# Performance work log

Hardware: AMD Instinct MI355X
Metric: run time of the kernel (lower is better)

Reference implementation:

```python
import jax, jax.numpy as jnp
import numpy as np

IN_FEATURES = 8192
OUT_FEATURES = 8192
W_BITS = 4
SCALE = float(2 ** 16)


def pbatch_round_quantize(W, n, scale=SCALE):
    """Faithful jnp port of pbatch_round_quantize.

    The torch module decomposes this quantized matrix into bitplanes packed
    into int32 words and accumulates scale_b * (bitplane @ x); the sum of the
    bitplane contributions is exactly (quantized / scale), so we compute that
    directly.
    """
    W_sign = jnp.sign(W)
    W_fixed = jnp.trunc(W * scale)            # (W * scale).astype(int), trunc toward 0
    v = jnp.abs(W_fixed)
    m = jnp.max(v)
    max_place = jnp.maximum(jnp.ceil(jnp.log2(m)) + 1.0, float(n))
    step = jnp.exp2(max_place - n)            # 2 ** (max_place - n)
    # mask = ((1<<max_place)-1) & ~(step-1) == 2**max_place - step
    mask = jnp.exp2(max_place) - step
    # bins[x] = mask - x*step (decreasing, uniformly spaced); centers are midpoints.
    # np.digitize(v, centers) for decreasing centers counts centers > v:
    #   idx = ceil((mask - v)/step - 0.5); then min(len(centers)-1, idx).
    if n == 1:
        # excl_zero: single bin, centers == bins, index always 0
        j = jnp.zeros_like(v)
    else:
        n_centers = 2 ** n - 1
        idx = jnp.ceil((mask - v) / step - 0.5)
        j = jnp.clip(idx, 0.0, float(n_centers - 1))
    rounded = W_sign * (mask - j * step)
    return rounded / scale


def setup_inputs() -> dict:
    key = jax.random.key(0)
    k_in, k_w, k_b = jax.random.split(key, 3)
    input = jax.random.normal(k_in, (IN_FEATURES,), dtype=jnp.float32)
    # reset_parameters: weight = randn(out, in)
    weight = jax.random.normal(k_w, (OUT_FEATURES, IN_FEATURES), dtype=jnp.float32)
    bound = 1.0 / np.sqrt(IN_FEATURES)
    bias = jax.random.uniform(k_b, (OUT_FEATURES,), dtype=jnp.float32,
                              minval=-bound, maxval=bound)
    return {"input": input, "weight": weight, "bias": bias}


def reference(input, weight, bias):
    # A_bits == 32 -> full-precision activations (no activation fixed-point path).
    Wq = pbatch_round_quantize(weight, W_BITS)       # [out, in]
    out = Wq @ input + bias                          # bit-serial GEMV result
    return out.reshape(1, -1)
```

## Files before the change

kernel.cpp:

```cpp
#include <hip/hip_runtime.h>

#define IN_F 8192
#define OUT_F 8192
#define NT 1024
#define VPT 2
#define RPB 32
#define NBLK (OUT_F / RPB)
#define NWAVE (NT / 64)

typedef float f32x4 __attribute__((ext_vector_type(4)));


__device__ __forceinline__ float qterm(float w, float xv, float inv_step, float& vmax) {
    float v = truncf(fabsf(w) * 65536.0f);
    vmax = fmaxf(vmax, v);
    float u = v * inv_step;
    float q = floorf(u + 0.5f);
    q = fminf(fmaxf(q, 1.0f), 15.0f);
    q = (w == 0.0f) ? 0.0f : q;
    float t = q * xv;
    return __uint_as_float(__float_as_uint(t) ^ (__float_as_uint(w) & 0x80000000u));
}

__global__ __launch_bounds__(NT, 4) void gemv_spec_kernel(
    const float* __restrict__ W, const float* __restrict__ x,
    const float* __restrict__ bias, float* __restrict__ out,
    unsigned* __restrict__ blkmax) {
    const int t = threadIdx.x;
    const int lane = t & 63, wid = t >> 6;
    const size_t row0 = (size_t)blockIdx.x * RPB;
    const f32x4* __restrict__ x4 = (const f32x4*)x;
    const float inv_step = 1.0f / 65536.0f;

    f32x4 xv[VPT];
#pragma unroll
    for (int k = 0; k < VPT; ++k) xv[k] = x4[t + NT * k];

    __shared__ float    ssum[RPB][NWAVE];
    __shared__ unsigned smax[NWAVE];
    float vmax = 0.0f;

#pragma unroll 2
    for (int j = 0; j < RPB; ++j) {
        const f32x4* __restrict__ Wr = (const f32x4*)(W + (row0 + j) * IN_F);
        f32x4 wv[VPT];
#pragma unroll
        for (int k = 0; k < VPT; ++k) wv[k] = Wr[t + NT * k];
        float a = 0.0f;
#pragma unroll
        for (int k = 0; k < VPT; ++k) {
            a += qterm(wv[k].x, xv[k].x, inv_step, vmax);
            a += qterm(wv[k].y, xv[k].y, inv_step, vmax);
            a += qterm(wv[k].z, xv[k].z, inv_step, vmax);
            a += qterm(wv[k].w, xv[k].w, inv_step, vmax);
        }
#pragma unroll
        for (int off = 32; off; off >>= 1) a += __shfl_down(a, off);
        if (lane == 0) ssum[j][wid] = a;
    }

#pragma unroll
    for (int off = 32; off; off >>= 1)
        vmax = fmaxf(vmax, __shfl_down(vmax, off));
    if (lane == 0) smax[wid] = __float_as_uint(vmax);
    __syncthreads();

    if (t < RPB) {
        float s = 0.0f;
#pragma unroll
        for (int wq = 0; wq < NWAVE; ++wq) s += ssum[t][wq];
        out[row0 + t] = s + bias[row0 + t];
    }
    if (t == NT - 1) {
        unsigned bm = 0u;
#pragma unroll
        for (int wq = 0; wq < NWAVE; ++wq) bm = max(bm, smax[wq]);
        blkmax[blockIdx.x] = bm;
    }
}

__global__ __launch_bounds__(256) void gemv_fix_kernel(
    const float* __restrict__ W, const float* __restrict__ x,
    const float* __restrict__ bias, float* __restrict__ out,
    const unsigned* __restrict__ blkmax) {
    const int t = threadIdx.x;
    const int lane = t & 63, wid = t >> 6;
    __shared__ unsigned sred[4];

    unsigned m = blkmax[t];
#pragma unroll
    for (int off = 32; off; off >>= 1)
        m = max(m, (unsigned)__shfl_down((int)m, off));
    if (lane == 0) sred[wid] = m;
    __syncthreads();
    m = max(max(sred[0], sred[1]), max(sred[2], sred[3]));
    const unsigned mi = (unsigned)__uint_as_float(m);

    int mp;
    if (mi <= 1u) mp = 1;
    else          mp = 33 - __clz((int)(mi - 1u));
    if (mp < 4) mp = 4;
    if (mp == 20) return;

    const float inv_step = __builtin_ldexpf(1.0f, 4 - mp);
    const float oscale   = __builtin_ldexpf(1.0f, mp - 20);
    const f32x4* __restrict__ x4 = (const f32x4*)x;

    f32x4 xv[8];
#pragma unroll
    for (int k = 0; k < 8; ++k) xv[k] = x4[t + 256 * k];

    __shared__ float ssum[4];
    float dummy = 0.0f;

    for (int r = 0; r < OUT_F; ++r) {
        const f32x4* __restrict__ Wr = (const f32x4*)(W + (size_t)r * IN_F);
        float a = 0.0f;
        for (int k = 0; k < 8; ++k) {
            f32x4 wv = Wr[t + 256 * k];
            a += qterm(wv.x, xv[k].x, inv_step, dummy);
            a += qterm(wv.y, xv[k].y, inv_step, dummy);
            a += qterm(wv.z, xv[k].z, inv_step, dummy);
            a += qterm(wv.w, xv[k].w, inv_step, dummy);
        }
#pragma unroll
        for (int off = 32; off; off >>= 1) a += __shfl_down(a, off);
        if (lane == 0) ssum[wid] = a;
        __syncthreads();
        if (t == 0)
            out[r] = (ssum[0] + ssum[1] + ssum[2] + ssum[3]) * oscale + bias[r];
        __syncthreads();
    }
}

extern "C" void kernel_launch(void* const* d_in, const int* in_sizes, int n_in,
                              void* d_out, int out_size, void* d_ws, size_t ws_size,
                              hipStream_t stream) {
    const float* x    = (const float*)d_in[0];
    const float* W    = (const float*)d_in[1];
    const float* bias = (const float*)d_in[2];
    float* out = (float*)d_out;
    unsigned* blkmax = (unsigned*)d_ws;

    gemv_spec_kernel<<<NBLK, NT, 0, stream>>>(W, x, bias, out, blkmax);
    gemv_fix_kernel<<<1, 256, 0, stream>>>(W, x, bias, out, blkmax);
}
```

Baseline: 44.71 us.

## Fuse speculative and fix-up GEMV kernels via cooperative grid sync

Merges the speculative quantized GEMV and the fallback kernel into one cooperative launch. A grid-wide sync makes every block wait until all per-block maxima are written. Each block then reduces the global maximum itself and, if the speculated quantization step was wrong, recomputes only its own 32 rows instead of one block redoing the whole matrix. This removes the second kernel launch and parallelises the fallback path. In exchange it adds a grid barrier and cooperative-launch overhead in the common case.

Measured after the change: 82.98 us. 85.6% more time.

```diff
diff --git a/kernel.cpp b/kernel.cpp
--- a/kernel.cpp
+++ b/kernel.cpp
@@ -1,4 +1,7 @@
 #include <hip/hip_runtime.h>
+#include <hip/hip_cooperative_groups.h>
+
+namespace cg = cooperative_groups;
 
 #define IN_F 8192
 #define OUT_F 8192
@@ -22,7 +25,7 @@
     return __uint_as_float(__float_as_uint(t) ^ (__float_as_uint(w) & 0x80000000u));
 }
 
-__global__ __launch_bounds__(NT, 4) void gemv_spec_kernel(
+__global__ __launch_bounds__(NT, 4) void gemv_fused_kernel(
     const float* __restrict__ W, const float* __restrict__ x,
     const float* __restrict__ bias, float* __restrict__ out,
     unsigned* __restrict__ blkmax) {
@@ -30,7 +33,7 @@
     const int lane = t & 63, wid = t >> 6;
     const size_t row0 = (size_t)blockIdx.x * RPB;
     const f32x4* __restrict__ x4 = (const f32x4*)x;
-    const float inv_step = 1.0f / 65536.0f;
+    const float inv_step0 = 1.0f / 65536.0f;
 
     f32x4 xv[VPT];
 #pragma unroll
@@ -38,6 +41,7 @@
 
     __shared__ float    ssum[RPB][NWAVE];
     __shared__ unsigned smax[NWAVE];
+    __shared__ unsigned sred[4];
     float vmax = 0.0f;
 
 #pragma unroll 2
@@ -49,10 +53,10 @@
         float a = 0.0f;
 #pragma unroll
         for (int k = 0; k < VPT; ++k) {
-            a += qterm(wv[k].x, xv[k].x, inv_step, vmax);
-            a += qterm(wv[k].y, xv[k].y, inv_step, vmax);
-            a += qterm(wv[k].z, xv[k].z, inv_step, vmax);
-            a += qterm(wv[k].w, xv[k].w, inv_step, vmax);
+            a += qterm(wv[k].x, xv[k].x, inv_step0, vmax);
+            a += qterm(wv[k].y, xv[k].y, inv_step0, vmax);
+            a += qterm(wv[k].z, xv[k].z, inv_step0, vmax);
+            a += qterm(wv[k].w, xv[k].w, inv_step0, vmax);
         }
 #pragma unroll
         for (int off = 32; off; off >>= 1) a += __shfl_down(a, off);
@@ -77,21 +81,14 @@
         for (int wq = 0; wq < NWAVE; ++wq) bm = max(bm, smax[wq]);
         blkmax[blockIdx.x] = bm;
     }
-}
 
-__global__ __launch_bounds__(256) void gemv_fix_kernel(
-    const float* __restrict__ W, const float* __restrict__ x,
-    const float* __restrict__ bias, float* __restrict__ out,
-    const unsigned* __restrict__ blkmax) {
-    const int t = threadIdx.x;
-    const int lane = t & 63, wid = t >> 6;
-    __shared__ unsigned sred[4];
+    cg::this_grid().sync();
 
-    unsigned m = blkmax[t];
+    unsigned m = (t < NBLK) ? blkmax[t] : 0u;
 #pragma unroll
     for (int off = 32; off; off >>= 1)
         m = max(m, (unsigned)__shfl_down((int)m, off));
-    if (lane == 0) sred[wid] = m;
+    if (t < NBLK && lane == 0) sred[wid] = m;
     __syncthreads();
     m = max(max(sred[0], sred[1]), max(sred[2], sred[3]));
     const unsigned mi = (unsigned)__uint_as_float(m);
@@ -104,20 +101,15 @@
 
     const float inv_step = __builtin_ldexpf(1.0f, 4 - mp);
     const float oscale   = __builtin_ldexpf(1.0f, mp - 20);
-    const f32x4* __restrict__ x4 = (const f32x4*)x;
+    float dummy = 0.0f;
+    __syncthreads();
 
-    f32x4 xv[8];
+    for (int j = 0; j < RPB; ++j) {
+        const f32x4* __restrict__ Wr = (const f32x4*)(W + (row0 + j) * IN_F);
+        float a = 0.0f;
 #pragma unroll
-    for (int k = 0; k < 8; ++k) xv[k] = x4[t + 256 * k];
-
-    __shared__ float ssum[4];
-    float dummy = 0.0f;
-
-    for (int r = 0; r < OUT_F; ++r) {
-        const f32x4* __restrict__ Wr = (const f32x4*)(W + (size_t)r * IN_F);
-        float a = 0.0f;
-        for (int k = 0; k < 8; ++k) {
-            f32x4 wv = Wr[t + 256 * k];
+        for (int k = 0; k < VPT; ++k) {
+            f32x4 wv = Wr[t + NT * k];
             a += qterm(wv.x, xv[k].x, inv_step, dummy);
             a += qterm(wv.y, xv[k].y, inv_step, dummy);
             a += qterm(wv.z, xv[k].z, inv_step, dummy);
@@ -125,11 +117,15 @@
         }
 #pragma unroll
         for (int off = 32; off; off >>= 1) a += __shfl_down(a, off);
-        if (lane == 0) ssum[wid] = a;
-        __syncthreads();
-        if (t == 0)
-            out[r] = (ssum[0] + ssum[1] + ssum[2] + ssum[3]) * oscale + bias[r];
-        __syncthreads();
+        if (lane == 0) ssum[j][wid] = a;
+    }
+    __syncthreads();
+
+    if (t < RPB) {
+        float s = 0.0f;
+#pragma unroll
+        for (int wq = 0; wq < NWAVE; ++wq) s += ssum[t][wq];
+        out[row0 + t] = s * oscale + bias[row0 + t];
     }
 }
 
@@ -142,6 +138,7 @@
     float* out = (float*)d_out;
     unsigned* blkmax = (unsigned*)d_ws;
 
-    gemv_spec_kernel<<<NBLK, NT, 0, stream>>>(W, x, bias, out, blkmax);
-    gemv_fix_kernel<<<1, 256, 0, stream>>>(W, x, bias, out, blkmax);
+    void* args[] = {(void*)&W, (void*)&x, (void*)&bias, (void*)&out, (void*)&blkmax};
+    hipLaunchCooperativeKernel((const void*)gemv_fused_kernel,
+                               dim3(NBLK), dim3(NT), args, 0, stream);
 }
```
